# Optimization experiments

Hardware: AMD Instinct MI355X
Metric: run time of the kernel (lower is better)

The kernel has to match this reference:

```python
import jax, jax.numpy as jnp
import numpy as np

T, B, I, H = 32, 8, 512, 512
CLIP = 1.0


def _softshrink(x, lambd=0.5):
    return jnp.where(x > lambd, x - lambd, jnp.where(x < -lambd, x + lambd, jnp.zeros_like(x)))


def setup_inputs() -> dict:
    key = jax.random.key(0)
    ks = jax.random.split(key, 5)
    sc = lambda k, sh, s: (s * jax.random.normal(k, sh)).astype(jnp.float32)
    return {
        "x": jax.random.normal(ks[0], (T, B, I), dtype=jnp.float32),
        "h0": jnp.zeros((B, H), jnp.float32),
        "v0": jnp.zeros((B, H), jnp.float32),
        "dU0": jnp.zeros((B, H, H), jnp.float32),
        "trace_e0": jnp.zeros((B, H), jnp.float32),
        "trace_E0": jnp.zeros((B, H, H), jnp.float32),
        "x2h_v": sc(ks[1], (3 * H, I), 0.05),
        "x2h_g": jnp.ones((3 * H,), jnp.float32),
        "x2h_b": jnp.zeros((3 * H,), jnp.float32),
        "h2h_v": sc(ks[2], (3 * H, H), 0.05),
        "h2h_g": jnp.ones((3 * H,), jnp.float32),
        "h2h_b": jnp.zeros((3 * H,), jnp.float32).at[:H].set(-1.0),
        "alpha": 0.1 * jnp.ones((1, H, H), jnp.float32),
        "h2mod_w": sc(ks[3], (4, H), 0.05),
        "h2mod_b": jnp.array([0.0, -2.0, -2.0, -3.0], jnp.float32),
        "modU_w": jnp.ones((1, H, H), jnp.float32),
        "modU_b": jnp.zeros((1, H, H), jnp.float32),
    }


def reference(x, h0, v0, dU0, trace_e0, trace_E0, x2h_v, x2h_g, x2h_b,
              h2h_v, h2h_g, h2h_b, alpha, h2mod_w, h2mod_b, modU_w, modU_b):
    Hd = h0.shape[-1]
    # weight_norm (dim=0): w[i,:] = g[i] * v[i,:] / ||v[i,:]||
    wn = lambda vv, g: g[:, None] * vv / jnp.linalg.norm(vv, axis=1, keepdims=True)
    Wx = wn(x2h_v, x2h_g)          # [3H, I]
    Wh = wn(h2h_v, h2h_g)          # [3H, H]
    # input projections for all timesteps at once
    xproj = jnp.einsum('tbi,oi->tbo', x, Wx) + x2h_b   # [T, B, 3H]
    Wr = Wh[Hd:2 * Hd]             # h2h.weight rows for r-gate, used in the dU clamp
    up = jax.nn.relu(CLIP - Wr) / (alpha + 1e-5)        # [1, H, H]
    lo = -jax.nn.relu(CLIP + Wr) / (alpha + 1e-5)       # [1, H, H]

    def step(carry, xp):
        h, v, dU, te, tE = carry
        hp = h @ Wh.T + h2h_b
        zx, rx, dvx = jnp.split(xp, 3, axis=-1)
        zh, rh, dvh = jnp.split(hp, 3, axis=-1)
        z = jax.nn.sigmoid(zx + zh)
        # NOTE: r = sigmoid(rx + rh) is computed in the original but never used in the update.
        dv = dvx + dvh + jnp.einsum('bij,bj->bi', alpha * dU, h)
        v_n = (1.0 - z) * v + z * dv
        hn = jax.nn.relu(v_n)                            # activation == 'relu'
        mod = hn @ h2mod_w.T + h2mod_b                   # [B, 4]
        tau_e = jax.nn.sigmoid(mod[:, 0:1])              # [B, 1]
        tau_E = jax.nn.sigmoid(mod[:, 1:2])[:, :, None]  # [B, 1, 1]
        tau_U = jax.nn.sigmoid(mod[:, 2:3])[:, :, None]  # [B, 1, 1]
        mU = jax.nn.relu(mod[:, 3:4])[:, :, None]        # [B, 1, 1]
        te_n = (1.0 - tau_e) * te + tau_e * h            # uses OLD h
        outer = hn[:, :, None] * te_n[:, None, :] - te_n[:, :, None] * hn[:, None, :]
        tE_n = (1.0 - tau_E) * tE + tau_E * outer
        dU_n = (1.0 - tau_U) * dU + tau_U * _softshrink(mU * modU_w + modU_b) * tE_n
        dU_n = jnp.clip(dU_n, lo, up)
        return (hn, v_n, dU_n, te_n, tE_n), hn

    (h, v, dU, te, tE), outs = jax.lax.scan(step, (h0, v0, dU0, trace_e0, trace_E0), xproj)
    return v, h, dU, te, tE, outs
```

## Files before the change

kernel.cpp:

```cpp
#include <hip/hip_runtime.h>
#include <math.h>


__device__ __forceinline__ float wred(float v) {
#pragma unroll
  for (int o = 32; o > 0; o >>= 1) v += __shfl_xor(v, o, 64);
  return v;
}
__device__ __forceinline__ float sigm(float x) { return 1.f / (1.f + __expf(-x)); }

__global__ void prenorm_kernel(const float* __restrict__ xv, const float* __restrict__ xg,
                               const float* __restrict__ hv, const float* __restrict__ hg,
                               float* __restrict__ scx, float* __restrict__ sch,
                               unsigned* __restrict__ flg) {
  int r = blockIdx.x, L = threadIdx.x;
  if (r < 16) {
#pragma unroll
    for (int k = 0; k < 8; k++) flg[r * 512 + k * 64 + L] = 0u;
  }
  const float* vrow; const float* g; float* o; int rr;
  if (r < 1536) { rr = r; vrow = xv + (size_t)r * 512; g = xg; o = scx; }
  else { rr = r - 1536; vrow = hv + (size_t)rr * 512; g = hg; o = sch; }
  float s = 0.f;
#pragma unroll
  for (int m = 0; m < 8; m++) { float v = vrow[m * 64 + L]; s = fmaf(v, v, s); }
  s = wred(s);
  if (L == 0) o[rr] = g[rr] / sqrtf(s);
}

__global__ __launch_bounds__(1024, 4) void persist_kernel(
    const float* __restrict__ x,
    const float* __restrict__ h0, const float* __restrict__ v0,
    const float* __restrict__ dU0, const float* __restrict__ te0,
    const float* __restrict__ tE0,
    const float* __restrict__ x2h_v, const float* __restrict__ x2h_b,
    const float* __restrict__ h2h_v, const float* __restrict__ h2h_b,
    const float* __restrict__ alpha,
    const float* __restrict__ h2mod_w, const float* __restrict__ h2mod_b,
    const float* __restrict__ modU_w, const float* __restrict__ modU_b,
    const float* __restrict__ scx, const float* __restrict__ sch,
    unsigned* __restrict__ flg,
    float* __restrict__ o_v, float* __restrict__ o_h,
    float* __restrict__ o_dU, float* __restrict__ o_te,
    float* __restrict__ o_tE, float* __restrict__ o_outs) {
  __shared__ float sh_hbuf[2][512];
  __shared__ float sh_te[512];
  __shared__ float sh_mod[2048];
  __shared__ float sh_xpz[32][16];
  __shared__ float sh_xpdv[32][16];
  __shared__ float sh_gates[4];

  const int tid = threadIdx.x;
  const int w = tid >> 6, L = tid & 63;
  const int b = blockIdx.x & 7, q = blockIdx.x >> 3;
  const int i = q * 16 + w;

  if (tid < 512) {
    sh_hbuf[0][tid] = h0[b * 512 + tid];
    sh_te[tid] = te0[b * 512 + tid];
  }
  sh_mod[tid] = h2mod_w[tid];
  sh_mod[tid + 1024] = h2mod_w[tid + 1024];

  const int rz = i, rdv = 1024 + i, rr = 512 + i;
  const size_t row  = ((size_t)(b * 512 + i)) * 512;
  const size_t wrow = (size_t)i * 512;

  {
    float xz[8], xdv[8];
    const float sx_z = scx[rz], sx_dv = scx[rdv];
#pragma unroll
    for (int m = 0; m < 8; m++) {
      int c = m * 64 + L;
      xz[m]  = sx_z  * x2h_v[(size_t)rz  * 512 + c];
      xdv[m] = sx_dv * x2h_v[(size_t)rdv * 512 + c];
    }
    float bz = 0.f, bdv = 0.f;
    if (L == 0) {
      bz  = x2h_b[i] + h2h_b[i];
      bdv = x2h_b[1024 + i] + h2h_b[1024 + i];
    }
#pragma unroll 4
    for (int t = 0; t < 32; t++) {
      const float* xr = x + (size_t)t * 4096 + b * 512;
      float a = 0.f, d = 0.f;
#pragma unroll
      for (int m = 0; m < 8; m++) {
        int c = m * 64 + L;
        float xv_ = xr[c];
        a = fmaf(xz[m], xv_, a);
        d = fmaf(xdv[m], xv_, d);
      }
      a = wred(a); d = wred(d);
      if (L == 0) { sh_xpz[t][w] = a + bz; sh_xpdv[t][w] = d + bdv; }
    }
  }

  float wz[8], wdv[8], mw[8], mb[8], al[8], upS[8], loS[8], D[8], tE[8];
  {
    const float s_z = sch[rz], s_dv = sch[rdv], s_r = sch[rr];
#pragma unroll
    for (int m = 0; m < 8; m++) {
      int c = m * 64 + L;
      wz[m]  = s_z  * h2h_v[(size_t)rz  * 512 + c];
      wdv[m] = s_dv * h2h_v[(size_t)rdv * 512 + c];
      mw[m] = modU_w[wrow + c];
      mb[m] = modU_b[wrow + c];
      float alv = alpha[wrow + c];
      al[m] = alv;
      float wrv = s_r * h2h_v[(size_t)rr * 512 + c];
      float t1 = alv / (alv + 1e-5f);
      upS[m] = fmaxf(1.f - wrv, 0.f) * t1;
      loS[m] = -fmaxf(1.f + wrv, 0.f) * t1;
      float dui = dU0[row + c];
      D[m]  = alv * dui;
      tE[m] = tE0[row + c];
    }
  }
  float v_reg = 0.f, hn_last = 0.f, gb = 0.f;
  if (L == 0) {
    v_reg = v0[b * 512 + i];
    if (w < 4) gb = h2mod_b[w];
  }
  __syncthreads();

  unsigned* hxu = (unsigned*)o_outs;

  for (int t = 0; t <= 32; t++) {
    const int cur = t & 1, prev = cur ^ 1;
    if (t > 0) {
      if (w == 0) {
        const unsigned* fp = flg + ((t - 1) * 8 + b) * 32 + (L & 31);
        unsigned u;
        do {
          u = __hip_atomic_load(fp, __ATOMIC_RELAXED, __HIP_MEMORY_SCOPE_AGENT);
        } while (!__all(u != 0u));
      }
      __syncthreads();
      if (tid < 512) {
        unsigned u = __hip_atomic_load(hxu + (size_t)(t - 1) * 4096 + b * 512 + tid,
                                       __ATOMIC_RELAXED, __HIP_MEMORY_SCOPE_AGENT);
        sh_hbuf[cur][tid] = __uint_as_float(u);
      }
      __syncthreads();
      if (w < 4) {
        float p = 0.f;
        const float* mr = sh_mod + w * 512;
#pragma unroll
        for (int m = 0; m < 8; m++) {
          int c = m * 64 + L;
          p = fmaf(sh_hbuf[cur][c], mr[c], p);
        }
        p = wred(p);
        if (L == 0) {
          p += gb;
          sh_gates[w] = (w == 3) ? fmaxf(p, 0.f) : sigm(p);
        }
      }
      __syncthreads();
      float taue = sh_gates[0];
      if (tid < 512) sh_te[tid] += taue * (sh_hbuf[prev][tid] - sh_te[tid]);
      __syncthreads();
      float tauE = sh_gates[1], tauU = sh_gates[2], mU = sh_gates[3];
      float hn_i = sh_hbuf[cur][i], te_i = sh_te[i];
#pragma unroll
      for (int m = 0; m < 8; m++) {
        int j = m * 64 + L;
        float outer = hn_i * sh_te[j] - te_i * sh_hbuf[cur][j];
        float tEn = tE[m] + tauE * (outer - tE[m]);
        float a = fmaf(mU, mw[m], mb[m]);
        float sshr = (a > 0.5f) ? (a - 0.5f) : ((a < -0.5f) ? (a + 0.5f) : 0.f);
        float Dn = D[m] + tauU * (sshr * (al[m] * tEn) - D[m]);
        D[m] = fminf(fmaxf(Dn, loS[m]), upS[m]);
        tE[m] = tEn;
      }
    }

    if (t < 32) {
      float p1 = 0.f, p2 = 0.f;
#pragma unroll
      for (int m = 0; m < 8; m++) {
        int c = m * 64 + L;
        float hc = sh_hbuf[cur][c];
        p1 = fmaf(wz[m], hc, p1);
        p2 = fmaf(wdv[m] + D[m], hc, p2);
      }
      p1 = wred(p1); p2 = wred(p2);
      if (L == 0) {
        float z = sigm(p1 + sh_xpz[t][w]);
        float dv = p2 + sh_xpdv[t][w];
        v_reg += z * (dv - v_reg);
        hn_last = fmaxf(v_reg, 0.f);
        __hip_atomic_store(hxu + (size_t)t * 4096 + b * 512 + i,
                           __float_as_uint(hn_last),
                           __ATOMIC_RELAXED, __HIP_MEMORY_SCOPE_AGENT);
      }
      __builtin_amdgcn_s_waitcnt(0);
      __syncthreads();
      if (tid == 0)
        __hip_atomic_store(flg + (t * 8 + b) * 32 + q, 1u,
                           __ATOMIC_RELAXED, __HIP_MEMORY_SCOPE_AGENT);
    }
  }

#pragma unroll
  for (int m = 0; m < 8; m++) {
    int c = m * 64 + L;
    float alv = al[m];
    o_dU[row + c] = (alv != 0.f) ? D[m] * __builtin_amdgcn_rcpf(alv) : 0.f;
    o_tE[row + c] = tE[m];
  }
  if (L == 0) {
    o_v[b * 512 + i] = v_reg;
    o_h[b * 512 + i] = hn_last;
  }
  if (q == 0 && tid < 512) o_te[b * 512 + tid] = sh_te[tid];
}

extern "C" void kernel_launch(void* const* d_in, const int* in_sizes, int n_in,
                              void* d_out, int out_size, void* d_ws, size_t ws_size,
                              hipStream_t stream) {
  const float* x       = (const float*)d_in[0];
  const float* h0      = (const float*)d_in[1];
  const float* v0      = (const float*)d_in[2];
  const float* dU0     = (const float*)d_in[3];
  const float* te0     = (const float*)d_in[4];
  const float* tE0     = (const float*)d_in[5];
  const float* x2h_v   = (const float*)d_in[6];
  const float* x2h_g   = (const float*)d_in[7];
  const float* x2h_b   = (const float*)d_in[8];
  const float* h2h_v   = (const float*)d_in[9];
  const float* h2h_g   = (const float*)d_in[10];
  const float* h2h_b   = (const float*)d_in[11];
  const float* alpha   = (const float*)d_in[12];
  const float* h2mod_w = (const float*)d_in[13];
  const float* h2mod_b = (const float*)d_in[14];
  const float* modU_w  = (const float*)d_in[15];
  const float* modU_b  = (const float*)d_in[16];

  float* out = (float*)d_out;
  float* o_v    = out;
  float* o_h    = out + 4096;
  float* o_dU   = out + 8192;
  float* o_te   = out + 2105344;
  float* o_tE   = out + 2109440;
  float* o_outs = out + 4206592;

  unsigned* flg = (unsigned*)d_ws;
  float* wsf = (float*)d_ws;
  float* scx = wsf + 8192;
  float* sch = wsf + 9728;

  prenorm_kernel<<<dim3(3072), dim3(64), 0, stream>>>(x2h_v, x2h_g, h2h_v, h2h_g,
                                                      scx, sch, flg);

  persist_kernel<<<dim3(256), dim3(1024), 0, stream>>>(
      x, h0, v0, dU0, te0, tE0, x2h_v, x2h_b, h2h_v, h2h_b, alpha,
      h2mod_w, h2mod_b, modU_w, modU_b, scx, sch, flg,
      o_v, o_h, o_dU, o_te, o_tE, o_outs);
}
```

Before: 278.1 us.

## Replace per-step flag barrier with sign-bit tagged h values and fused update

```diff
diff --git a/kernel.cpp b/kernel.cpp
--- a/kernel.cpp
+++ b/kernel.cpp
@@ -1,6 +1,9 @@
 #include <hip/hip_runtime.h>
 #include <math.h>
 
+
+#define ATOMIC_LD(p) __hip_atomic_load((p), __ATOMIC_RELAXED, __HIP_MEMORY_SCOPE_AGENT)
+#define ATOMIC_ST(p, v) __hip_atomic_store((p), (v), __ATOMIC_RELAXED, __HIP_MEMORY_SCOPE_AGENT)
 
 __device__ __forceinline__ float wred(float v) {
 #pragma unroll
@@ -12,12 +15,10 @@
 __global__ void prenorm_kernel(const float* __restrict__ xv, const float* __restrict__ xg,
                                const float* __restrict__ hv, const float* __restrict__ hg,
                                float* __restrict__ scx, float* __restrict__ sch,
-                               unsigned* __restrict__ flg) {
+                               unsigned* __restrict__ outs_u, unsigned* __restrict__ done) {
   int r = blockIdx.x, L = threadIdx.x;
-  if (r < 16) {
-#pragma unroll
-    for (int k = 0; k < 8; k++) flg[r * 512 + k * 64 + L] = 0u;
-  }
+  if (r < 2048) outs_u[r * 64 + L] = 0u;
+  if (r == 2048 && L < 8) done[L] = 0u;
   const float* vrow; const float* g; float* o; int rr;
   if (r < 1536) { rr = r; vrow = xv + (size_t)r * 512; g = xg; o = scx; }
   else { rr = r - 1536; vrow = hv + (size_t)rr * 512; g = hg; o = sch; }
@@ -39,26 +40,23 @@
     const float* __restrict__ h2mod_w, const float* __restrict__ h2mod_b,
     const float* __restrict__ modU_w, const float* __restrict__ modU_b,
     const float* __restrict__ scx, const float* __restrict__ sch,
-    unsigned* __restrict__ flg,
+    unsigned* __restrict__ done,
     float* __restrict__ o_v, float* __restrict__ o_h,
     float* __restrict__ o_dU, float* __restrict__ o_te,
     float* __restrict__ o_tE, float* __restrict__ o_outs) {
-  __shared__ float sh_hbuf[2][512];
-  __shared__ float sh_te[512];
+  __shared__ float sh_h[3][512];
   __shared__ float sh_mod[2048];
+  __shared__ float sh_mw[16][512];
   __shared__ float sh_xpz[32][16];
   __shared__ float sh_xpdv[32][16];
-  __shared__ float sh_gates[4];
+  __shared__ float sh_gates[2][4];
 
   const int tid = threadIdx.x;
   const int w = tid >> 6, L = tid & 63;
   const int b = blockIdx.x & 7, q = blockIdx.x >> 3;
   const int i = q * 16 + w;
 
-  if (tid < 512) {
-    sh_hbuf[0][tid] = h0[b * 512 + tid];
-    sh_te[tid] = te0[b * 512 + tid];
-  }
+  if (tid < 512) sh_h[0][tid] = h0[b * 512 + tid];
   sh_mod[tid] = h2mod_w[tid];
   sh_mod[tid + 1024] = h2mod_w[tid + 1024];
 
@@ -96,7 +94,7 @@
     }
   }
 
-  float wz[8], wdv[8], mw[8], mb[8], al[8], upS[8], loS[8], D[8], tE[8];
+  float wz[8], wdv[8], mb[8], al[8], upS[8], loS[8], D[8], tE[8], te[8];
   {
     const float s_z = sch[rz], s_dv = sch[rdv], s_r = sch[rr];
 #pragma unroll
@@ -104,7 +102,7 @@
       int c = m * 64 + L;
       wz[m]  = s_z  * h2h_v[(size_t)rz  * 512 + c];
       wdv[m] = s_dv * h2h_v[(size_t)rdv * 512 + c];
-      mw[m] = modU_w[wrow + c];
+      sh_mw[w][c] = modU_w[wrow + c];
       mb[m] = modU_b[wrow + c];
       float alv = alpha[wrow + c];
       al[m] = alv;
@@ -112,94 +110,92 @@
       float t1 = alv / (alv + 1e-5f);
       upS[m] = fmaxf(1.f - wrv, 0.f) * t1;
       loS[m] = -fmaxf(1.f + wrv, 0.f) * t1;
-      float dui = dU0[row + c];
-      D[m]  = alv * dui;
+      D[m]  = alv * dU0[row + c];
       tE[m] = tE0[row + c];
-    }
-  }
-  float v_reg = 0.f, hn_last = 0.f, gb = 0.f;
-  if (L == 0) {
-    v_reg = v0[b * 512 + i];
-    if (w < 4) gb = h2mod_b[w];
-  }
+      te[m] = te0[b * 512 + c];
+    }
+  }
+  float v_reg    = v0[b * 512 + i];
+  float h_cur_i  = h0[b * 512 + i];
+  float h_prev_i = 0.f;
+  float te_i     = te0[b * 512 + i];
+  float gb = (w < 4) ? h2mod_b[w] : 0.f;
   __syncthreads();
 
   unsigned* hxu = (unsigned*)o_outs;
-
-  for (int t = 0; t <= 32; t++) {
-    const int cur = t & 1, prev = cur ^ 1;
+  int cur = 0;
+
+  for (int t = 0; t <= 32; ++t) {
+    const int prevslot = cur;
     if (t > 0) {
-      if (w == 0) {
-        const unsigned* fp = flg + ((t - 1) * 8 + b) * 32 + (L & 31);
+      cur = (cur == 2) ? 0 : cur + 1;
+      const unsigned* hsrc = hxu + (size_t)(t - 1) * 4096 + b * 512;
+      if (w < 4) {
+        unsigned u[8];
+        for (;;) {
+          bool ok = true;
+#pragma unroll
+          for (int m = 0; m < 8; m++) u[m] = ATOMIC_LD(hsrc + m * 64 + L);
+#pragma unroll
+          for (int m = 0; m < 8; m++) ok = ok && ((u[m] >> 31) != 0u);
+          if (ok) break;
+        }
+        float gp = 0.f;
+#pragma unroll
+        for (int m = 0; m < 8; m++)
+          gp = fmaf(__uint_as_float(u[m] & 0x7fffffffu),
+                    sh_mod[w * 512 + m * 64 + L], gp);
+        gp = wred(gp) + gb;
+        if (L == 0) sh_gates[t & 1][w] = (w == 3) ? fmaxf(gp, 0.f) : sigm(gp);
+      } else if (w < 12) {
+        const int j = tid - 256;
         unsigned u;
-        do {
-          u = __hip_atomic_load(fp, __ATOMIC_RELAXED, __HIP_MEMORY_SCOPE_AGENT);
-        } while (!__all(u != 0u));
-      }
-      __syncthreads();
-      if (tid < 512) {
-        unsigned u = __hip_atomic_load(hxu + (size_t)(t - 1) * 4096 + b * 512 + tid,
-                                       __ATOMIC_RELAXED, __HIP_MEMORY_SCOPE_AGENT);
-        sh_hbuf[cur][tid] = __uint_as_float(u);
-      }
-      __syncthreads();
-      if (w < 4) {
-        float p = 0.f;
-        const float* mr = sh_mod + w * 512;
-#pragma unroll
-        for (int m = 0; m < 8; m++) {
-          int c = m * 64 + L;
-          p = fmaf(sh_hbuf[cur][c], mr[c], p);
-        }
-        p = wred(p);
-        if (L == 0) {
-          p += gb;
-          sh_gates[w] = (w == 3) ? fmaxf(p, 0.f) : sigm(p);
-        }
-      }
-      __syncthreads();
-      float taue = sh_gates[0];
-      if (tid < 512) sh_te[tid] += taue * (sh_hbuf[prev][tid] - sh_te[tid]);
-      __syncthreads();
-      float tauE = sh_gates[1], tauU = sh_gates[2], mU = sh_gates[3];
-      float hn_i = sh_hbuf[cur][i], te_i = sh_te[i];
-#pragma unroll
-      for (int m = 0; m < 8; m++) {
-        int j = m * 64 + L;
-        float outer = hn_i * sh_te[j] - te_i * sh_hbuf[cur][j];
-        float tEn = tE[m] + tauE * (outer - tE[m]);
-        float a = fmaf(mU, mw[m], mb[m]);
-        float sshr = (a > 0.5f) ? (a - 0.5f) : ((a < -0.5f) ? (a + 0.5f) : 0.f);
-        float Dn = D[m] + tauU * (sshr * (al[m] * tEn) - D[m]);
-        D[m] = fminf(fmaxf(Dn, loS[m]), upS[m]);
-        tE[m] = tEn;
-      }
-    }
-
-    if (t < 32) {
-      float p1 = 0.f, p2 = 0.f;
+        do { u = ATOMIC_LD(hsrc + j); } while (!(u >> 31));
+        sh_h[cur][j] = __uint_as_float(u & 0x7fffffffu);
+      }
+    }
+    __syncthreads();
+
+    float p1 = 0.f, p2 = 0.f;
+    if (t > 0) {
+      const float taue = sh_gates[t & 1][0], tauE = sh_gates[t & 1][1];
+      const float tauU = sh_gates[t & 1][2], mU   = sh_gates[t & 1][3];
+      te_i += taue * (h_prev_i - te_i);
 #pragma unroll
       for (int m = 0; m < 8; m++) {
         int c = m * 64 + L;
-        float hc = sh_hbuf[cur][c];
-        p1 = fmaf(wz[m], hc, p1);
-        p2 = fmaf(wdv[m] + D[m], hc, p2);
-      }
+        float hcm = sh_h[cur][c];
+        float hpm = sh_h[prevslot][c];
+        te[m] += taue * (hpm - te[m]);
+        float outer = h_cur_i * te[m] - te_i * hcm;
+        tE[m] += tauE * (outer - tE[m]);
+        float a = fmaf(mU, sh_mw[w][c], mb[m]);
+        float sshr = (a > 0.5f) ? (a - 0.5f) : ((a < -0.5f) ? (a + 0.5f) : 0.f);
+        float Dn = D[m] + tauU * (sshr * (al[m] * tE[m]) - D[m]);
+        D[m] = fminf(fmaxf(Dn, loS[m]), upS[m]);
+        p1 = fmaf(wz[m], hcm, p1);
+        p2 = fmaf(wdv[m] + D[m], hcm, p2);
+      }
+    } else {
+#pragma unroll
+      for (int m = 0; m < 8; m++) {
+        float hcm = sh_h[0][m * 64 + L];
+        p1 = fmaf(wz[m], hcm, p1);
+        p2 = fmaf(wdv[m] + D[m], hcm, p2);
+      }
+    }
+
+    if (t < 32) {
       p1 = wred(p1); p2 = wred(p2);
-      if (L == 0) {
-        float z = sigm(p1 + sh_xpz[t][w]);
-        float dv = p2 + sh_xpdv[t][w];
-        v_reg += z * (dv - v_reg);
-        hn_last = fmaxf(v_reg, 0.f);
-        __hip_atomic_store(hxu + (size_t)t * 4096 + b * 512 + i,
-                           __float_as_uint(hn_last),
-                           __ATOMIC_RELAXED, __HIP_MEMORY_SCOPE_AGENT);
-      }
-      __builtin_amdgcn_s_waitcnt(0);
-      __syncthreads();
-      if (tid == 0)
-        __hip_atomic_store(flg + (t * 8 + b) * 32 + q, 1u,
-                           __ATOMIC_RELAXED, __HIP_MEMORY_SCOPE_AGENT);
+      float z  = sigm(p1 + sh_xpz[t][w]);
+      float dv = p2 + sh_xpdv[t][w];
+      v_reg += z * (dv - v_reg);
+      float hn = fmaxf(v_reg, 0.f);
+      if (L == 0)
+        ATOMIC_ST(hxu + (size_t)t * 4096 + b * 512 + i,
+                  __float_as_uint(hn) | 0x80000000u);
+      h_prev_i = h_cur_i;
+      h_cur_i  = hn;
     }
   }
 
@@ -210,11 +206,25 @@
     o_dU[row + c] = (alv != 0.f) ? D[m] * __builtin_amdgcn_rcpf(alv) : 0.f;
     o_tE[row + c] = tE[m];
   }
-  if (L == 0) {
-    o_v[b * 512 + i] = v_reg;
-    o_h[b * 512 + i] = hn_last;
-  }
-  if (q == 0 && tid < 512) o_te[b * 512 + tid] = sh_te[tid];
+  if (L == 0) { o_v[b * 512 + i] = v_reg; o_h[b * 512 + i] = h_cur_i; }
+  if (q == 0 && w == 0) {
+#pragma unroll
+    for (int m = 0; m < 8; m++) o_te[b * 512 + m * 64 + L] = te[m];
+  }
+
+  __syncthreads();
+  if (tid == 0)
+    __hip_atomic_fetch_add(done + b, 1u, __ATOMIC_RELAXED, __HIP_MEMORY_SCOPE_AGENT);
+  if (w == 0) {
+    unsigned c;
+    do { c = ATOMIC_LD(done + b); } while (c < 32u);
+  }
+  __syncthreads();
+  if (tid < 512) {
+    int tt = tid >> 4, r2 = tid & 15;
+    unsigned* p = hxu + (size_t)tt * 4096 + b * 512 + q * 16 + r2;
+    ATOMIC_ST(p, ATOMIC_LD(p) & 0x7fffffffu);
+  }
 }
 
 extern "C" void kernel_launch(void* const* d_in, const int* in_sizes, int n_in,
@@ -246,16 +256,16 @@
   float* o_tE   = out + 2109440;
   float* o_outs = out + 4206592;
 
-  unsigned* flg = (unsigned*)d_ws;
+  unsigned* done = (unsigned*)d_ws;
   float* wsf = (float*)d_ws;
   float* scx = wsf + 8192;
   float* sch = wsf + 9728;
 
-  prenorm_kernel<<<dim3(3072), dim3(64), 0, stream>>>(x2h_v, x2h_g, h2h_v, h2h_g,
-                                                      scx, sch, flg);
+  prenorm_kernel<<<dim3(3072), dim3(64), 0, stream>>>(
+      x2h_v, x2h_g, h2h_v, h2h_g, scx, sch, (unsigned*)o_outs, done);
 
   persist_kernel<<<dim3(256), dim3(1024), 0, stream>>>(
       x, h0, v0, dU0, te0, tE0, x2h_v, x2h_b, h2h_v, h2h_b, alpha,
-      h2mod_w, h2mod_b, modU_w, modU_b, scx, sch, flg,
+      h2mod_w, h2mod_b, modU_w, modU_b, scx, sch, done,
       o_v, o_h, o_dU, o_te, o_tE, o_outs);
 }
```

New measurement: 374.1 us. +34.5%, slower.

## Replace flag-plus-data handshake with self-validating tagged hidden-state exchange

Applied to the files above, without the earlier changes.

```diff
diff --git a/kernel.cpp b/kernel.cpp
--- a/kernel.cpp
+++ b/kernel.cpp
@@ -1,6 +1,9 @@
 #include <hip/hip_runtime.h>
 #include <math.h>
 
+
+#define ATOMIC_LD(p) __hip_atomic_load((p), __ATOMIC_RELAXED, __HIP_MEMORY_SCOPE_AGENT)
+#define ATOMIC_ST(p, v) __hip_atomic_store((p), (v), __ATOMIC_RELAXED, __HIP_MEMORY_SCOPE_AGENT)
 
 __device__ __forceinline__ float wred(float v) {
 #pragma unroll
@@ -12,12 +15,9 @@
 __global__ void prenorm_kernel(const float* __restrict__ xv, const float* __restrict__ xg,
                                const float* __restrict__ hv, const float* __restrict__ hg,
                                float* __restrict__ scx, float* __restrict__ sch,
-                               unsigned* __restrict__ flg) {
+                               unsigned* __restrict__ exch) {
   int r = blockIdx.x, L = threadIdx.x;
-  if (r < 16) {
-#pragma unroll
-    for (int k = 0; k < 8; k++) flg[r * 512 + k * 64 + L] = 0u;
-  }
+  if (r < 2048) exch[r * 64 + L] = 0u;
   const float* vrow; const float* g; float* o; int rr;
   if (r < 1536) { rr = r; vrow = xv + (size_t)r * 512; g = xg; o = scx; }
   else { rr = r - 1536; vrow = hv + (size_t)rr * 512; g = hg; o = sch; }
@@ -39,7 +39,7 @@
     const float* __restrict__ h2mod_w, const float* __restrict__ h2mod_b,
     const float* __restrict__ modU_w, const float* __restrict__ modU_b,
     const float* __restrict__ scx, const float* __restrict__ sch,
-    unsigned* __restrict__ flg,
+    unsigned* __restrict__ exch,
     float* __restrict__ o_v, float* __restrict__ o_h,
     float* __restrict__ o_dU, float* __restrict__ o_te,
     float* __restrict__ o_tE, float* __restrict__ o_outs) {
@@ -49,6 +49,7 @@
   __shared__ float sh_xpz[32][16];
   __shared__ float sh_xpdv[32][16];
   __shared__ float sh_gates[4];
+  __shared__ float sh_gather[16];
 
   const int tid = threadIdx.x;
   const int w = tid >> 6, L = tid & 63;
@@ -124,23 +125,22 @@
   }
   __syncthreads();
 
-  unsigned* hxu = (unsigned*)o_outs;
-
   for (int t = 0; t <= 32; t++) {
     const int cur = t & 1, prev = cur ^ 1;
     if (t > 0) {
+      const unsigned* eb = exch + ((t - 1) * 8 + b) * 512;
       if (w == 0) {
-        const unsigned* fp = flg + ((t - 1) * 8 + b) * 32 + (L & 31);
+        const unsigned* fp = eb + (L & 31) * 16 + (L & 15);
         unsigned u;
         do {
-          u = __hip_atomic_load(fp, __ATOMIC_RELAXED, __HIP_MEMORY_SCOPE_AGENT);
-        } while (!__all(u != 0u));
+          u = ATOMIC_LD(fp);
+        } while (!__all(u >> 31));
       }
       __syncthreads();
       if (tid < 512) {
-        unsigned u = __hip_atomic_load(hxu + (size_t)(t - 1) * 4096 + b * 512 + tid,
-                                       __ATOMIC_RELAXED, __HIP_MEMORY_SCOPE_AGENT);
-        sh_hbuf[cur][tid] = __uint_as_float(u);
+        unsigned u = ATOMIC_LD(eb + tid);
+        while (!(u >> 31)) u = ATOMIC_LD(eb + tid);
+        sh_hbuf[cur][tid] = __uint_as_float(u & 0x7fffffffu);
       }
       __syncthreads();
       if (w < 4) {
@@ -191,15 +191,14 @@
         float dv = p2 + sh_xpdv[t][w];
         v_reg += z * (dv - v_reg);
         hn_last = fmaxf(v_reg, 0.f);
-        __hip_atomic_store(hxu + (size_t)t * 4096 + b * 512 + i,
-                           __float_as_uint(hn_last),
-                           __ATOMIC_RELAXED, __HIP_MEMORY_SCOPE_AGENT);
-      }
-      __builtin_amdgcn_s_waitcnt(0);
-      __syncthreads();
-      if (tid == 0)
-        __hip_atomic_store(flg + (t * 8 + b) * 32 + q, 1u,
-                           __ATOMIC_RELAXED, __HIP_MEMORY_SCOPE_AGENT);
+        o_outs[(size_t)t * 4096 + b * 512 + i] = hn_last;
+        sh_gather[w] = hn_last;
+      }
+      __syncthreads();
+      if (w == 15 && L < 16) {
+        unsigned u = __float_as_uint(sh_gather[L]) | 0x80000000u;
+        ATOMIC_ST(exch + (t * 8 + b) * 512 + q * 16 + L, u);
+      }
     }
   }
 
@@ -246,16 +245,16 @@
   float* o_tE   = out + 2109440;
   float* o_outs = out + 4206592;
 
-  unsigned* flg = (unsigned*)d_ws;
   float* wsf = (float*)d_ws;
   float* scx = wsf + 8192;
   float* sch = wsf + 9728;
+  unsigned* exch = (unsigned*)d_ws + 12288;
 
   prenorm_kernel<<<dim3(3072), dim3(64), 0, stream>>>(x2h_v, x2h_g, h2h_v, h2h_g,
-                                                      scx, sch, flg);
+                                                      scx, sch, exch);
 
   persist_kernel<<<dim3(256), dim3(1024), 0, stream>>>(
       x, h0, v0, dU0, te0, tE0, x2h_v, x2h_b, h2h_v, h2h_b, alpha,
-      h2mod_w, h2mod_b, modU_w, modU_b, scx, sch, flg,
+      h2mod_w, h2mod_b, modU_w, modU_b, scx, sch, exch,
       o_v, o_h, o_dU, o_te, o_tE, o_outs);
 }
```

Result: faster. 246.5 us (median of 2 runs) (-11.4%).
